# Kernel tuning notes

Measured on AMD Instinct MI355X. Metric: run time of the kernel, lower is better.

## Reference

```python
import jax, jax.numpy as jnp
import numpy as np

ALPHA = 0.2  # LeakyReLU negative slope
N1, N2, D_IN, D_OUT = 4096, 8192, 256, 256


def _xavier(key, shape):
    fan_in, fan_out = shape[0], shape[1]
    std = 1.414 * (2.0 / (fan_in + fan_out)) ** 0.5
    return (jax.random.normal(key, shape) * std).astype(jnp.float32)


def setup_inputs() -> dict:
    key = jax.random.key(0)
    k1, k2, k3, k4, k5 = jax.random.split(key, 5)
    x = jax.random.normal(k1, (N2, D_IN), dtype=jnp.float32)
    adj = (jax.random.uniform(k2, (N1, N2)) < 0.01).astype(jnp.float32)
    adj = adj.at[:, 0].set(1.0)
    weight_v2e = _xavier(k3, (D_IN, D_OUT))
    weight_e2v = _xavier(k4, (D_OUT, D_OUT))
    a = _xavier(k5, (1, 2 * D_OUT))
    return {"x": x, "adj": adj, "weight_v2e": weight_v2e, "weight_e2v": weight_e2v, "a": a}


def reference(x, adj, weight_v2e, weight_e2v, a):
    out = weight_v2e.shape[1]
    x_4att = x @ weight_v2e                              # [N2, out]
    degree = jnp.sum(adj, axis=1, keepdims=True)         # [N1, 1]
    edge = (adj @ x_4att) / degree                       # [N1, out] mean of incident node feats
    edge_4att = edge @ weight_e2v                        # [N1, out]
    # score(i,j) = a . concat(x_4att[j], edge_4att[i]); decomposes additively
    a_node = a[0, :out]                                  # applied to x_4att
    a_edge = a[0, out:]                                  # applied to edge_4att
    scores = edge_4att @ a_edge                          # [N1]
    scores = scores[:, None] + (x_4att @ a_node)[None, :]  # [N1, N2]
    pair_e = jax.nn.leaky_relu(scores, negative_slope=ALPHA)
    attention = jnp.where(adj > 0, pair_e, jnp.float32(-9e15))
    attention_node = jax.nn.softmax(attention.T, axis=1)  # [N2, N1] softmax over hyperedges per node
    node = attention_node @ edge_4att                    # [N2, out]
    return jax.nn.leaky_relu(node, negative_slope=ALPHA)
```

## Files before the change

kernel.cpp:

```cpp
#include <hip/hip_runtime.h>
#include <math.h>


#define N1 4096
#define N2 8192
#define D  256
#define ALPHA 0.2f
#define CCAP 96

__global__ void __launch_bounds__(256) prep_kernel(
    const float* __restrict__ Wv, const float* __restrict__ We,
    const float* __restrict__ a, float* __restrict__ Wf,
    float* __restrict__ vnode, float* __restrict__ vedge,
    float* __restrict__ c0num, float* __restrict__ c0den,
    int* __restrict__ colcnt)
{
    __shared__ float tmp[256];
    const int t = threadIdx.x;
    const int b = blockIdx.x;
    if (b < 256) {
        float acc = 0.f;
        for (int m = 0; m < 256; ++m)
            acc += Wv[b * 256 + m] * We[m * 256 + t];
        Wf[b * 256 + t] = acc;
    } else if (b == 256) {
        float acc = 0.f;
        for (int n = 0; n < 256; ++n)
            acc += Wv[t * 256 + n] * a[n];
        vnode[t] = acc;
        float t2 = 0.f;
        for (int n = 0; n < 256; ++n)
            t2 += We[t * 256 + n] * a[256 + n];
        tmp[t] = t2;
        __syncthreads();
        float v = 0.f;
        for (int n = 0; n < 256; ++n)
            v += Wv[t * 256 + n] * tmp[n];
        vedge[t] = v;
    } else {
        c0num[t] = 0.f;
        if (t == 0) *c0den = 0.f;
        for (int u = 0; u < 32; ++u) colcnt[u * 256 + t] = 0;
    }
}

__global__ void __launch_bounds__(512) edge_mean_kernel(
    const float* __restrict__ adj, const float* __restrict__ x,
    const float* __restrict__ vedge, float* __restrict__ ex,
    float* __restrict__ sr, int* __restrict__ colcnt,
    unsigned short* __restrict__ colidx)
{
    __shared__ int    lst[512];
    __shared__ int    cnt;
    __shared__ float4 part[7][64];
    const int t = threadIdx.x, lane = t & 63, w = t >> 6;
    const int i = blockIdx.x;
    if (t == 0) cnt = 0;
    __syncthreads();

    const float4* arow = (const float4*)(adj + (size_t)i * N2);
    for (int u = 0; u < 4; ++u) {
        const float4 v = arow[u * 512 + t];
        const int jb = (u * 512 + t) * 4;
        const float comp[4] = {v.x, v.y, v.z, v.w};
#pragma unroll
        for (int q = 0; q < 4; ++q) {
            if (comp[q] != 0.f) {
                const int k = atomicAdd(&cnt, 1);
                if (k < 512) lst[k] = jb + q;
            }
        }
    }
    __syncthreads();
    const int deg = cnt;
    const int c = deg < 512 ? deg : 512;

    for (int k = t; k < c; k += 512) {
        const int j = lst[k];
        if (j != 0) {
            const int kk = atomicAdd(&colcnt[j], 1);
            if (kk < CCAP) colidx[(size_t)j * CCAP + kk] = (unsigned short)i;
        }
    }

    const float4* x4 = (const float4*)x;
    float4 acc = {0.f, 0.f, 0.f, 0.f};
    float4 acc2 = {0.f, 0.f, 0.f, 0.f};
    int k = w;
    for (; k + 56 < c; k += 64) {
        const int j0 = lst[k],      j1 = lst[k + 8],  j2 = lst[k + 16], j3 = lst[k + 24];
        const int j4 = lst[k + 32], j5 = lst[k + 40], j6 = lst[k + 48], j7 = lst[k + 56];
        const float4 v0 = x4[(size_t)j0 * 64 + lane];
        const float4 v1 = x4[(size_t)j1 * 64 + lane];
        const float4 v2 = x4[(size_t)j2 * 64 + lane];
        const float4 v3 = x4[(size_t)j3 * 64 + lane];
        const float4 v4 = x4[(size_t)j4 * 64 + lane];
        const float4 v5 = x4[(size_t)j5 * 64 + lane];
        const float4 v6 = x4[(size_t)j6 * 64 + lane];
        const float4 v7 = x4[(size_t)j7 * 64 + lane];
        acc.x  += (v0.x + v1.x) + (v2.x + v3.x);
        acc.y  += (v0.y + v1.y) + (v2.y + v3.y);
        acc.z  += (v0.z + v1.z) + (v2.z + v3.z);
        acc.w  += (v0.w + v1.w) + (v2.w + v3.w);
        acc2.x += (v4.x + v5.x) + (v6.x + v7.x);
        acc2.y += (v4.y + v5.y) + (v6.y + v7.y);
        acc2.z += (v4.z + v5.z) + (v6.z + v7.z);
        acc2.w += (v4.w + v5.w) + (v6.w + v7.w);
    }
    for (; k + 8 < c; k += 16) {
        const float4 v0 = x4[(size_t)lst[k] * 64 + lane];
        const float4 v1 = x4[(size_t)lst[k + 8] * 64 + lane];
        acc.x += v0.x;  acc.y += v0.y;  acc.z += v0.z;  acc.w += v0.w;
        acc2.x += v1.x; acc2.y += v1.y; acc2.z += v1.z; acc2.w += v1.w;
    }
    for (; k < c; k += 8) {
        const float4 v = x4[(size_t)lst[k] * 64 + lane];
        acc.x += v.x; acc.y += v.y; acc.z += v.z; acc.w += v.w;
    }
    acc.x += acc2.x; acc.y += acc2.y; acc.z += acc2.z; acc.w += acc2.w;

    if (w > 0) part[w - 1][lane] = acc;
    __syncthreads();

    if (w == 0) {
        float4 s = acc;
#pragma unroll
        for (int p = 0; p < 7; ++p) {
            const float4 q = part[p][lane];
            s.x += q.x; s.y += q.y; s.z += q.z; s.w += q.w;
        }
        const float invd = 1.0f / (float)(deg > 0 ? deg : 1);
        float4 e = {s.x * invd, s.y * invd, s.z * invd, s.w * invd};
        ((float4*)(ex + (size_t)i * D))[lane] = e;

        const float4 ve = ((const float4*)vedge)[lane];
        float p = e.x * ve.x + e.y * ve.y + e.z * ve.z + e.w * ve.w;
#pragma unroll
        for (int off = 32; off >= 1; off >>= 1) p += __shfl_xor(p, off, 64);
        if (lane == 0) sr[i] = p;
    }
}

__global__ void __launch_bounds__(256) gemm16_kernel(
    float* __restrict__ exe, const float* __restrict__ Wf)
{
    __shared__ float exl[16 * 256];
    __shared__ float Wfl[64 * 256];
    const int t = threadIdx.x;
    const int r0 = blockIdx.x * 16;

    for (int r = 0; r < 16; ++r)
        exl[r * 256 + t] = exe[(size_t)(r0 + r) * D + t];

    float acc[16];
#pragma unroll
    for (int r = 0; r < 16; ++r) acc[r] = 0.f;

    for (int p = 0; p < 4; ++p) {
        __syncthreads();
        const float4* Wg = (const float4*)(Wf + p * 64 * 256);
        float4* Wd = (float4*)Wfl;
        for (int u = 0; u < 16; ++u)
            Wd[u * 256 + t] = Wg[u * 256 + t];
        __syncthreads();
        for (int n = 0; n < 64; ++n) {
            const float wl = Wfl[n * 256 + t];
#pragma unroll
            for (int r = 0; r < 16; ++r)
                acc[r] += exl[r * 256 + p * 64 + n] * wl;
        }
    }
#pragma unroll
    for (int r = 0; r < 16; ++r)
        exe[(size_t)(r0 + r) * D + t] = acc[r];
}

__global__ void __launch_bounds__(512) attn_kernel(
    const float* __restrict__ x, const float* __restrict__ vnode,
    const float* __restrict__ sr, const float* __restrict__ e4a,
    const int* __restrict__ colcnt, const unsigned short* __restrict__ colidx,
    float* __restrict__ out)
{
    const int t = threadIdx.x, lane = t & 63, w = t >> 6;
    const int j = blockIdx.x * 8 + w;
    if (j == 0) return;
    const float4 vn = *(const float4*)(vnode + lane * 4);
    const float4* e44 = (const float4*)e4a;

    const float4 xu = *(const float4*)(x + (size_t)j * D + lane * 4);
    float p = xu.x * vn.x + xu.y * vn.y + xu.z * vn.z + xu.w * vn.w;
#pragma unroll
    for (int off = 32; off >= 1; off >>= 1) p += __shfl_xor(p, off, 64);
    const float sc = p;

    int c = colcnt[j]; if (c > CCAP) c = CCAP;
    const unsigned short* lp = colidx + (size_t)j * CCAP;

    int   id0 = 0,  id1 = 0;
    float wk0 = 0.f, wk1 = 0.f;
    if (lane < c) {
        id0 = lp[lane];
        float s = sr[id0] + sc;
        s = s > 0.f ? s : ALPHA * s;
        wk0 = __expf(s);
    }
    if (lane + 64 < c) {
        id1 = lp[lane + 64];
        float s = sr[id1] + sc;
        s = s > 0.f ? s : ALPHA * s;
        wk1 = __expf(s);
    }
    float den = wk0 + wk1;
#pragma unroll
    for (int off = 32; off >= 1; off >>= 1) den += __shfl_xor(den, off, 64);

    float4 acc = {0.f, 0.f, 0.f, 0.f};
    float4 accB = {0.f, 0.f, 0.f, 0.f};
    const int c1 = c < 64 ? c : 64;
    int k = 0;
    for (; k + 7 < c1; k += 8) {
        const int   i0 = __shfl(id0, k, 64),     i1 = __shfl(id0, k + 1, 64);
        const int   i2 = __shfl(id0, k + 2, 64), i3 = __shfl(id0, k + 3, 64);
        const int   i4 = __shfl(id0, k + 4, 64), i5 = __shfl(id0, k + 5, 64);
        const int   i6 = __shfl(id0, k + 6, 64), i7 = __shfl(id0, k + 7, 64);
        const float w0 = __shfl(wk0, k, 64),     w1 = __shfl(wk0, k + 1, 64);
        const float w2 = __shfl(wk0, k + 2, 64), w3 = __shfl(wk0, k + 3, 64);
        const float w4 = __shfl(wk0, k + 4, 64), w5 = __shfl(wk0, k + 5, 64);
        const float w6 = __shfl(wk0, k + 6, 64), w7 = __shfl(wk0, k + 7, 64);
        const float4 v0 = e44[(size_t)i0 * 64 + lane];
        const float4 v1 = e44[(size_t)i1 * 64 + lane];
        const float4 v2 = e44[(size_t)i2 * 64 + lane];
        const float4 v3 = e44[(size_t)i3 * 64 + lane];
        const float4 v4 = e44[(size_t)i4 * 64 + lane];
        const float4 v5 = e44[(size_t)i5 * 64 + lane];
        const float4 v6 = e44[(size_t)i6 * 64 + lane];
        const float4 v7 = e44[(size_t)i7 * 64 + lane];
        acc.x  += w0 * v0.x + w1 * v1.x + w2 * v2.x + w3 * v3.x;
        acc.y  += w0 * v0.y + w1 * v1.y + w2 * v2.y + w3 * v3.y;
        acc.z  += w0 * v0.z + w1 * v1.z + w2 * v2.z + w3 * v3.z;
        acc.w  += w0 * v0.w + w1 * v1.w + w2 * v2.w + w3 * v3.w;
        accB.x += w4 * v4.x + w5 * v5.x + w6 * v6.x + w7 * v7.x;
        accB.y += w4 * v4.y + w5 * v5.y + w6 * v6.y + w7 * v7.y;
        accB.z += w4 * v4.z + w5 * v5.z + w6 * v6.z + w7 * v7.z;
        accB.w += w4 * v4.w + w5 * v5.w + w6 * v6.w + w7 * v7.w;
    }
    for (; k < c1; ++k) {
        const int   idx = __shfl(id0, k, 64);
        const float wt  = __shfl(wk0, k, 64);
        const float4 v = e44[(size_t)idx * 64 + lane];
        acc.x += wt * v.x; acc.y += wt * v.y; acc.z += wt * v.z; acc.w += wt * v.w;
    }
    for (k = 64; k < c; ++k) {
        const int   idx = __shfl(id1, k - 64, 64);
        const float wt  = __shfl(wk1, k - 64, 64);
        const float4 v = e44[(size_t)idx * 64 + lane];
        accB.x += wt * v.x; accB.y += wt * v.y; accB.z += wt * v.z; accB.w += wt * v.w;
    }
    acc.x += accB.x; acc.y += accB.y; acc.z += accB.z; acc.w += accB.w;

    const float dinv = den > 0.f ? 1.0f / den : 0.f;
    float n0 = acc.x * dinv, n1 = acc.y * dinv, n2 = acc.z * dinv, n3 = acc.w * dinv;
    n0 = n0 > 0.f ? n0 : ALPHA * n0;
    n1 = n1 > 0.f ? n1 : ALPHA * n1;
    n2 = n2 > 0.f ? n2 : ALPHA * n2;
    n3 = n3 > 0.f ? n3 : ALPHA * n3;
    const float4 o = {n0, n1, n2, n3};
    *(float4*)(out + (size_t)j * D + lane * 4) = o;
}

__global__ void __launch_bounds__(256) col0_partial_kernel(
    const float* __restrict__ x, const float* __restrict__ vnode,
    const float* __restrict__ sr, const float* __restrict__ e4a,
    float* __restrict__ c0num, float* __restrict__ c0den)
{
    __shared__ float red[256];
    __shared__ float wl[16];
    const int t = threadIdx.x;
    const int r0 = blockIdx.x * 16;

    red[t] = x[t] * vnode[t];
    __syncthreads();
    for (int s = 128; s > 0; s >>= 1) {
        if (t < s) red[t] += red[t + s];
        __syncthreads();
    }
    const float sc0 = red[0];
    __syncthreads();

    if (t < 16) {
        float s = sr[r0 + t] + sc0;
        s = s > 0.f ? s : ALPHA * s;
        wl[t] = __expf(s);
    }
    __syncthreads();

    float num = 0.f;
#pragma unroll
    for (int r = 0; r < 16; ++r)
        num += wl[r] * e4a[(size_t)(r0 + r) * D + t];
    atomicAdd(&c0num[t], num);
    if (t == 0) {
        float ds = 0.f;
#pragma unroll
        for (int r = 0; r < 16; ++r) ds += wl[r];
        atomicAdd(c0den, ds);
    }
}

__global__ void __launch_bounds__(256) col0_final_kernel(
    const float* __restrict__ c0num, const float* __restrict__ c0den,
    float* __restrict__ out)
{
    const int t = threadIdx.x;
    const float d = *c0den;
    float v = d > 0.f ? c0num[t] / d : 0.f;
    out[t] = v > 0.f ? v : ALPHA * v;
}

extern "C" void kernel_launch(void* const* d_in, const int* in_sizes, int n_in,
                              void* d_out, int out_size, void* d_ws, size_t ws_size,
                              hipStream_t stream)
{
    const float* x   = (const float*)d_in[0];
    const float* adj = (const float*)d_in[1];
    const float* Wv  = (const float*)d_in[2];
    const float* We  = (const float*)d_in[3];
    const float* a   = (const float*)d_in[4];

    char* ws = (char*)d_ws;
    float*          exe4a  = (float*)(ws);
    float*          sr     = (float*)(ws + 0x400000);
    float*          Wf     = (float*)(ws + 0x404000);
    float*          vnode  = (float*)(ws + 0x444000);
    float*          vedge  = (float*)(ws + 0x444400);
    float*          c0num  = (float*)(ws + 0x444800);
    float*          c0den  = (float*)(ws + 0x444C00);
    int*            colcnt = (int*)(ws + 0x444D00);
    unsigned short* colidx = (unsigned short*)(ws + 0x44CD00);

    prep_kernel<<<dim3(258), dim3(256), 0, stream>>>(Wv, We, a, Wf, vnode, vedge,
                                                     c0num, c0den, colcnt);
    edge_mean_kernel<<<dim3(N1), dim3(512), 0, stream>>>(adj, x, vedge, exe4a, sr,
                                                         colcnt, colidx);
    gemm16_kernel<<<dim3(N1 / 16), dim3(256), 0, stream>>>(exe4a, Wf);
    attn_kernel<<<dim3(N2 / 8), dim3(512), 0, stream>>>(x, vnode, sr, exe4a,
                                                        colcnt, colidx, (float*)d_out);
    col0_partial_kernel<<<dim3(256), dim3(256), 0, stream>>>(x, vnode, sr, exe4a,
                                                             c0num, c0den);
    col0_final_kernel<<<dim3(1), dim3(256), 0, stream>>>(c0num, c0den, (float*)d_out);
}
```

Baseline: 308.6 us.

## Split adjacency scan from edge gather and use wave-ballot compaction

The fused edge-mean kernel is split into a lightweight scan kernel that compacts each adjacency row's nonzero indices into a global row list, and a gather kernel that reads that list and averages x rows. The scan uses wavefront ballot/popcount to replace per-element shared atomics with one atomic per wave, and does the column-index atomics inline. The intent is to cut shared-atomic contention and let the bandwidth-bound scan and the gather run at separate occupancy. The cost is an extra launch plus writing and reading the row index list through global memory.

```diff
diff --git a/kernel.cpp b/kernel.cpp
--- a/kernel.cpp
+++ b/kernel.cpp
@@ -7,6 +7,7 @@
 #define D  256
 #define ALPHA 0.2f
 #define CCAP 96
+#define RCAP 512
 
 __global__ void __launch_bounds__(256) prep_kernel(
     const float* __restrict__ Wv, const float* __restrict__ We,
@@ -44,44 +45,64 @@
     }
 }
 
-__global__ void __launch_bounds__(512) edge_mean_kernel(
-    const float* __restrict__ adj, const float* __restrict__ x,
-    const float* __restrict__ vedge, float* __restrict__ ex,
-    float* __restrict__ sr, int* __restrict__ colcnt,
+__global__ void __launch_bounds__(256) scan_kernel(
+    const float* __restrict__ adj, int* __restrict__ rowcnt,
+    unsigned short* __restrict__ rowidx, int* __restrict__ colcnt,
     unsigned short* __restrict__ colidx)
 {
-    __shared__ int    lst[512];
-    __shared__ int    cnt;
+    __shared__ int cnt;
+    const int t = threadIdx.x, lane = t & 63;
+    const int i = blockIdx.x;
+    if (t == 0) cnt = 0;
+    __syncthreads();
+
+    const float4* arow = (const float4*)(adj + (size_t)i * N2);
+    unsigned short* rp = rowidx + (size_t)i * RCAP;
+
+    for (int u = 0; u < 8; ++u) {
+        const float4 v = arow[u * 256 + t];
+        const int jb = (u * 256 + t) * 4;
+        const float comp[4] = {v.x, v.y, v.z, v.w};
+#pragma unroll
+        for (int q = 0; q < 4; ++q) {
+            const bool nz = (comp[q] != 0.f);
+            const unsigned long long m = __ballot(nz);
+            if (m) {
+                int base = 0;
+                if (lane == 0) base = atomicAdd(&cnt, __popcll(m));
+                base = __shfl(base, 0, 64);
+                if (nz) {
+                    const int j = jb + q;
+                    const int pos = base +
+                        __popcll(m & ((1ull << lane) - 1ull));
+                    if (pos < RCAP) rp[pos] = (unsigned short)j;
+                    if (j != 0) {
+                        const int kk = atomicAdd(&colcnt[j], 1);
+                        if (kk < CCAP)
+                            colidx[(size_t)j * CCAP + kk] = (unsigned short)i;
+                    }
+                }
+            }
+        }
+    }
+    __syncthreads();
+    if (t == 0) rowcnt[i] = cnt;
+}
+
+__global__ void __launch_bounds__(512) edge_gather_kernel(
+    const float* __restrict__ x, const int* __restrict__ rowcnt,
+    const unsigned short* __restrict__ rowidx, const float* __restrict__ vedge,
+    float* __restrict__ ex, float* __restrict__ sr)
+{
+    __shared__ unsigned short lst[RCAP];
     __shared__ float4 part[7][64];
     const int t = threadIdx.x, lane = t & 63, w = t >> 6;
     const int i = blockIdx.x;
-    if (t == 0) cnt = 0;
-    __syncthreads();
-
-    const float4* arow = (const float4*)(adj + (size_t)i * N2);
-    for (int u = 0; u < 4; ++u) {
-        const float4 v = arow[u * 512 + t];
-        const int jb = (u * 512 + t) * 4;
-        const float comp[4] = {v.x, v.y, v.z, v.w};
-#pragma unroll
-        for (int q = 0; q < 4; ++q) {
-            if (comp[q] != 0.f) {
-                const int k = atomicAdd(&cnt, 1);
-                if (k < 512) lst[k] = jb + q;
-            }
-        }
-    }
-    __syncthreads();
-    const int deg = cnt;
-    const int c = deg < 512 ? deg : 512;
-
-    for (int k = t; k < c; k += 512) {
-        const int j = lst[k];
-        if (j != 0) {
-            const int kk = atomicAdd(&colcnt[j], 1);
-            if (kk < CCAP) colidx[(size_t)j * CCAP + kk] = (unsigned short)i;
-        }
-    }
+
+    const int deg = rowcnt[i];
+    const int c = deg < RCAP ? deg : RCAP;
+    if (t < c) lst[t] = rowidx[(size_t)i * RCAP + t];
+    __syncthreads();
 
     const float4* x4 = (const float4*)x;
     float4 acc = {0.f, 0.f, 0.f, 0.f};
@@ -337,11 +358,15 @@
     float*          c0den  = (float*)(ws + 0x444C00);
     int*            colcnt = (int*)(ws + 0x444D00);
     unsigned short* colidx = (unsigned short*)(ws + 0x44CD00);
+    int*            rowcnt = (int*)(ws + 0x5CCD00);
+    unsigned short* rowidx = (unsigned short*)(ws + 0x5D0D00);
 
     prep_kernel<<<dim3(258), dim3(256), 0, stream>>>(Wv, We, a, Wf, vnode, vedge,
                                                      c0num, c0den, colcnt);
-    edge_mean_kernel<<<dim3(N1), dim3(512), 0, stream>>>(adj, x, vedge, exe4a, sr,
-                                                         colcnt, colidx);
+    scan_kernel<<<dim3(N1), dim3(256), 0, stream>>>(adj, rowcnt, rowidx,
+                                                    colcnt, colidx);
+    edge_gather_kernel<<<dim3(N1), dim3(512), 0, stream>>>(x, rowcnt, rowidx,
+                                                           vedge, exe4a, sr);
     gemm16_kernel<<<dim3(N1 / 16), dim3(256), 0, stream>>>(exe4a, Wf);
     attn_kernel<<<dim3(N2 / 8), dim3(512), 0, stream>>>(x, vnode, sr, exe4a,
                                                         colcnt, colidx, (float*)d_out);
```

After: 332.4 us. +7.7%, slower.

## Replace sparse column gather attention with dense bf16 MFMA GEMM over adjacency

Applied to the files above, without the earlier changes.

Drops the per-column sparse index lists (colcnt/colidx built with atomics), the separate column-0 path and the per-node gather of edge features. The node aggregation becomes a dense GEMM: softmax weights are computed on the fly from the adjacency tile, packed to bf16, and multiplied against a transposed bf16 copy of edge_4att with MFMA 16x16x32 instructions, with the denominator accumulated in shared memory. This re-reads the full 128MB adjacency and does dense work over roughly 99% zeros, and it adds bf16 rounding error, in exchange for regular, tensor-core-friendly access.

```diff
diff --git a/kernel.cpp b/kernel.cpp
--- a/kernel.cpp
+++ b/kernel.cpp
@@ -6,14 +6,20 @@
 #define N2 8192
 #define D  256
 #define ALPHA 0.2f
-#define CCAP 96
+
+typedef __attribute__((ext_vector_type(8))) short short8;
+typedef __attribute__((ext_vector_type(4))) float floatx4;
+
+__device__ __forceinline__ unsigned short f2b(float f) {
+    unsigned int x = __float_as_uint(f);
+    x += 0x7FFFu + ((x >> 16) & 1u);
+    return (unsigned short)(x >> 16);
+}
 
 __global__ void __launch_bounds__(256) prep_kernel(
     const float* __restrict__ Wv, const float* __restrict__ We,
     const float* __restrict__ a, float* __restrict__ Wf,
-    float* __restrict__ vnode, float* __restrict__ vedge,
-    float* __restrict__ c0num, float* __restrict__ c0den,
-    int* __restrict__ colcnt)
+    float* __restrict__ vnode, float* __restrict__ vedge)
 {
     __shared__ float tmp[256];
     const int t = threadIdx.x;
@@ -23,7 +29,7 @@
         for (int m = 0; m < 256; ++m)
             acc += Wv[b * 256 + m] * We[m * 256 + t];
         Wf[b * 256 + t] = acc;
-    } else if (b == 256) {
+    } else {
         float acc = 0.f;
         for (int n = 0; n < 256; ++n)
             acc += Wv[t * 256 + n] * a[n];
@@ -37,18 +43,13 @@
         for (int n = 0; n < 256; ++n)
             v += Wv[t * 256 + n] * tmp[n];
         vedge[t] = v;
-    } else {
-        c0num[t] = 0.f;
-        if (t == 0) *c0den = 0.f;
-        for (int u = 0; u < 32; ++u) colcnt[u * 256 + t] = 0;
     }
 }
 
 __global__ void __launch_bounds__(512) edge_mean_kernel(
     const float* __restrict__ adj, const float* __restrict__ x,
     const float* __restrict__ vedge, float* __restrict__ ex,
-    float* __restrict__ sr, int* __restrict__ colcnt,
-    unsigned short* __restrict__ colidx)
+    float* __restrict__ sr)
 {
     __shared__ int    lst[512];
     __shared__ int    cnt;
@@ -74,14 +75,6 @@
     __syncthreads();
     const int deg = cnt;
     const int c = deg < 512 ? deg : 512;
-
-    for (int k = t; k < c; k += 512) {
-        const int j = lst[k];
-        if (j != 0) {
-            const int kk = atomicAdd(&colcnt[j], 1);
-            if (kk < CCAP) colidx[(size_t)j * CCAP + kk] = (unsigned short)i;
-        }
-    }
 
     const float4* x4 = (const float4*)x;
     float4 acc = {0.f, 0.f, 0.f, 0.f};
@@ -142,7 +135,8 @@
 }
 
 __global__ void __launch_bounds__(256) gemm16_kernel(
-    float* __restrict__ exe, const float* __restrict__ Wf)
+    const float* __restrict__ ex, const float* __restrict__ Wf,
+    unsigned short* __restrict__ e4aT)
 {
     __shared__ float exl[16 * 256];
     __shared__ float Wfl[64 * 256];
@@ -150,7 +144,7 @@
     const int r0 = blockIdx.x * 16;
 
     for (int r = 0; r < 16; ++r)
-        exl[r * 256 + t] = exe[(size_t)(r0 + r) * D + t];
+        exl[r * 256 + t] = ex[(size_t)(r0 + r) * D + t];
 
     float acc[16];
 #pragma unroll
@@ -170,151 +164,134 @@
                 acc[r] += exl[r * 256 + p * 64 + n] * wl;
         }
     }
-#pragma unroll
-    for (int r = 0; r < 16; ++r)
-        exe[(size_t)(r0 + r) * D + t] = acc[r];
-}
-
-__global__ void __launch_bounds__(512) attn_kernel(
+    unsigned short pk[16];
+#pragma unroll
+    for (int r = 0; r < 16; ++r) pk[r] = f2b(acc[r]);
+    unsigned short* dst = e4aT + (size_t)t * N1 + r0;
+    *(uint4*)(dst)     = *(const uint4*)(&pk[0]);
+    *(uint4*)(dst + 8) = *(const uint4*)(&pk[8]);
+}
+
+__global__ void __launch_bounds__(512) sc_kernel(
     const float* __restrict__ x, const float* __restrict__ vnode,
-    const float* __restrict__ sr, const float* __restrict__ e4a,
-    const int* __restrict__ colcnt, const unsigned short* __restrict__ colidx,
-    float* __restrict__ out)
+    float* __restrict__ sc)
 {
     const int t = threadIdx.x, lane = t & 63, w = t >> 6;
     const int j = blockIdx.x * 8 + w;
-    if (j == 0) return;
     const float4 vn = *(const float4*)(vnode + lane * 4);
-    const float4* e44 = (const float4*)e4a;
-
     const float4 xu = *(const float4*)(x + (size_t)j * D + lane * 4);
     float p = xu.x * vn.x + xu.y * vn.y + xu.z * vn.z + xu.w * vn.w;
 #pragma unroll
     for (int off = 32; off >= 1; off >>= 1) p += __shfl_xor(p, off, 64);
-    const float sc = p;
-
-    int c = colcnt[j]; if (c > CCAP) c = CCAP;
-    const unsigned short* lp = colidx + (size_t)j * CCAP;
-
-    int   id0 = 0,  id1 = 0;
-    float wk0 = 0.f, wk1 = 0.f;
-    if (lane < c) {
-        id0 = lp[lane];
-        float s = sr[id0] + sc;
-        s = s > 0.f ? s : ALPHA * s;
-        wk0 = __expf(s);
-    }
-    if (lane + 64 < c) {
-        id1 = lp[lane + 64];
-        float s = sr[id1] + sc;
-        s = s > 0.f ? s : ALPHA * s;
-        wk1 = __expf(s);
-    }
-    float den = wk0 + wk1;
-#pragma unroll
-    for (int off = 32; off >= 1; off >>= 1) den += __shfl_xor(den, off, 64);
-
-    float4 acc = {0.f, 0.f, 0.f, 0.f};
-    float4 accB = {0.f, 0.f, 0.f, 0.f};
-    const int c1 = c < 64 ? c : 64;
-    int k = 0;
-    for (; k + 7 < c1; k += 8) {
-        const int   i0 = __shfl(id0, k, 64),     i1 = __shfl(id0, k + 1, 64);
-        const int   i2 = __shfl(id0, k + 2, 64), i3 = __shfl(id0, k + 3, 64);
-        const int   i4 = __shfl(id0, k + 4, 64), i5 = __shfl(id0, k + 5, 64);
-        const int   i6 = __shfl(id0, k + 6, 64), i7 = __shfl(id0, k + 7, 64);
-        const float w0 = __shfl(wk0, k, 64),     w1 = __shfl(wk0, k + 1, 64);
-        const float w2 = __shfl(wk0, k + 2, 64), w3 = __shfl(wk0, k + 3, 64);
-        const float w4 = __shfl(wk0, k + 4, 64), w5 = __shfl(wk0, k + 5, 64);
-        const float w6 = __shfl(wk0, k + 6, 64), w7 = __shfl(wk0, k + 7, 64);
-        const float4 v0 = e44[(size_t)i0 * 64 + lane];
-        const float4 v1 = e44[(size_t)i1 * 64 + lane];
-        const float4 v2 = e44[(size_t)i2 * 64 + lane];
-        const float4 v3 = e44[(size_t)i3 * 64 + lane];
-        const float4 v4 = e44[(size_t)i4 * 64 + lane];
-        const float4 v5 = e44[(size_t)i5 * 64 + lane];
-        const float4 v6 = e44[(size_t)i6 * 64 + lane];
-        const float4 v7 = e44[(size_t)i7 * 64 + lane];
-        acc.x  += w0 * v0.x + w1 * v1.x + w2 * v2.x + w3 * v3.x;
-        acc.y  += w0 * v0.y + w1 * v1.y + w2 * v2.y + w3 * v3.y;
-        acc.z  += w0 * v0.z + w1 * v1.z + w2 * v2.z + w3 * v3.z;
-        acc.w  += w0 * v0.w + w1 * v1.w + w2 * v2.w + w3 * v3.w;
-        accB.x += w4 * v4.x + w5 * v5.x + w6 * v6.x + w7 * v7.x;
-        accB.y += w4 * v4.y + w5 * v5.y + w6 * v6.y + w7 * v7.y;
-        accB.z += w4 * v4.z + w5 * v5.z + w6 * v6.z + w7 * v7.z;
-        accB.w += w4 * v4.w + w5 * v5.w + w6 * v6.w + w7 * v7.w;
-    }
-    for (; k < c1; ++k) {
-        const int   idx = __shfl(id0, k, 64);
-        const float wt  = __shfl(wk0, k, 64);
-        const float4 v = e44[(size_t)idx * 64 + lane];
-        acc.x += wt * v.x; acc.y += wt * v.y; acc.z += wt * v.z; acc.w += wt * v.w;
-    }
-    for (k = 64; k < c; ++k) {
-        const int   idx = __shfl(id1, k - 64, 64);
-        const float wt  = __shfl(wk1, k - 64, 64);
-        const float4 v = e44[(size_t)idx * 64 + lane];
-        accB.x += wt * v.x; accB.y += wt * v.y; accB.z += wt * v.z; accB.w += wt * v.w;
-    }
-    acc.x += accB.x; acc.y += accB.y; acc.z += accB.z; acc.w += accB.w;
-
-    const float dinv = den > 0.f ? 1.0f / den : 0.f;
-    float n0 = acc.x * dinv, n1 = acc.y * dinv, n2 = acc.z * dinv, n3 = acc.w * dinv;
-    n0 = n0 > 0.f ? n0 : ALPHA * n0;
-    n1 = n1 > 0.f ? n1 : ALPHA * n1;
-    n2 = n2 > 0.f ? n2 : ALPHA * n2;
-    n3 = n3 > 0.f ? n3 : ALPHA * n3;
-    const float4 o = {n0, n1, n2, n3};
-    *(float4*)(out + (size_t)j * D + lane * 4) = o;
-}
-
-__global__ void __launch_bounds__(256) col0_partial_kernel(
-    const float* __restrict__ x, const float* __restrict__ vnode,
-    const float* __restrict__ sr, const float* __restrict__ e4a,
-    float* __restrict__ c0num, float* __restrict__ c0den)
-{
-    __shared__ float red[256];
-    __shared__ float wl[16];
-    const int t = threadIdx.x;
-    const int r0 = blockIdx.x * 16;
-
-    red[t] = x[t] * vnode[t];
-    __syncthreads();
-    for (int s = 128; s > 0; s >>= 1) {
-        if (t < s) red[t] += red[t + s];
-        __syncthreads();
-    }
-    const float sc0 = red[0];
-    __syncthreads();
-
-    if (t < 16) {
-        float s = sr[r0 + t] + sc0;
-        s = s > 0.f ? s : ALPHA * s;
-        wl[t] = __expf(s);
-    }
-    __syncthreads();
-
-    float num = 0.f;
-#pragma unroll
-    for (int r = 0; r < 16; ++r)
-        num += wl[r] * e4a[(size_t)(r0 + r) * D + t];
-    atomicAdd(&c0num[t], num);
-    if (t == 0) {
-        float ds = 0.f;
-#pragma unroll
-        for (int r = 0; r < 16; ++r) ds += wl[r];
-        atomicAdd(c0den, ds);
-    }
-}
-
-__global__ void __launch_bounds__(256) col0_final_kernel(
-    const float* __restrict__ c0num, const float* __restrict__ c0den,
+    if (lane == 0) sc[j] = p;
+}
+
+__global__ void __launch_bounds__(512) gemm2_kernel(
+    const float* __restrict__ adj, const float* __restrict__ sr,
+    const float* __restrict__ sc, const unsigned short* __restrict__ e4aT,
     float* __restrict__ out)
 {
-    const int t = threadIdx.x;
-    const float d = *c0den;
-    float v = d > 0.f ? c0num[t] / d : 0.f;
-    out[t] = v > 0.f ? v : ALPHA * v;
+    __shared__ unsigned short A_w[32 * 64];
+    __shared__ unsigned short BT[256 * 64];
+    __shared__ float scl[32];
+    __shared__ float den_l[32];
+    const int t = threadIdx.x, lane = t & 63, w = t >> 6;
+    const int j0 = blockIdx.x * 32;
+
+    if (t < 32) { scl[t] = sc[j0 + t]; den_l[t] = 0.f; }
+
+    const int jown   = t & 31;
+    const int islice = t >> 5;
+    const int iq     = islice >> 1;
+    const int ebase  = (islice & 1) * 4;
+    float den_reg = 0.f;
+
+    const int bc   = t >> 1;
+    const int bh   = t & 1;
+
+    floatx4 acc0 = {0.f,0.f,0.f,0.f}, acc1 = {0.f,0.f,0.f,0.f};
+    floatx4 acc2 = {0.f,0.f,0.f,0.f}, acc3 = {0.f,0.f,0.f,0.f};
+
+    const int mt  = w & 1;
+    const int nt0 = (w >> 1) * 4;
+    const int fm  = mt * 16 + (lane & 15);
+    const int fl7 = lane & 7;
+    const int fq  = lane >> 4;
+
+    __syncthreads();
+
+    for (int kt = 0; kt < 64; ++kt) {
+        const int k0 = kt * 64;
+
+        {
+            const float scj = scl[jown];
+            unsigned short pk[4];
+#pragma unroll
+            for (int u = 0; u < 4; ++u) {
+                const int i = islice * 4 + u;
+                const float av = adj[(size_t)(k0 + i) * N2 + j0 + jown];
+                float wv = 0.f;
+                if (av != 0.f) {
+                    float s = sr[k0 + i] + scj;
+                    s = s > 0.f ? s : ALPHA * s;
+                    s = fminf(fmaxf(s, -60.f), 60.f);
+                    wv = __expf(s);
+                }
+                den_reg += wv;
+                pk[u] = f2b(wv);
+            }
+            *(ushort4*)&A_w[jown * 64 + (iq ^ (jown & 7)) * 8 + ebase] =
+                *(const ushort4*)pk;
+        }
+        {
+            const unsigned short* src = e4aT + (size_t)bc * N1 + k0 + bh * 32;
+            unsigned short* drow = &BT[bc * 64];
+            const int c7 = bc & 7;
+#pragma unroll
+            for (int m = 0; m < 4; ++m) {
+                const uint4 v = *(const uint4*)(src + m * 8);
+                *(uint4*)&drow[((bh * 4 + m) ^ c7) * 8] = v;
+            }
+        }
+        __syncthreads();
+
+#pragma unroll
+        for (int step = 0; step < 2; ++step) {
+            const int kq = step * 4 + fq;
+            const short8 af =
+                *(const short8*)&A_w[fm * 64 + (kq ^ fl7) * 8];
+            const short8 b0 =
+                *(const short8*)&BT[((nt0 + 0) * 16 + (lane & 15)) * 64 + (kq ^ fl7) * 8];
+            const short8 b1 =
+                *(const short8*)&BT[((nt0 + 1) * 16 + (lane & 15)) * 64 + (kq ^ fl7) * 8];
+            const short8 b2 =
+                *(const short8*)&BT[((nt0 + 2) * 16 + (lane & 15)) * 64 + (kq ^ fl7) * 8];
+            const short8 b3 =
+                *(const short8*)&BT[((nt0 + 3) * 16 + (lane & 15)) * 64 + (kq ^ fl7) * 8];
+            acc0 = __builtin_amdgcn_mfma_f32_16x16x32_bf16(af, b0, acc0, 0, 0, 0);
+            acc1 = __builtin_amdgcn_mfma_f32_16x16x32_bf16(af, b1, acc1, 0, 0, 0);
+            acc2 = __builtin_amdgcn_mfma_f32_16x16x32_bf16(af, b2, acc2, 0, 0, 0);
+            acc3 = __builtin_amdgcn_mfma_f32_16x16x32_bf16(af, b3, acc3, 0, 0, 0);
+        }
+        __syncthreads();
+    }
+
+    atomicAdd(&den_l[jown], den_reg);
+    __syncthreads();
+
+    const floatx4 accs[4] = {acc0, acc1, acc2, acc3};
+#pragma unroll
+    for (int p = 0; p < 4; ++p) {
+        const int cg = (nt0 + p) * 16 + (lane & 15);
+#pragma unroll
+        for (int r = 0; r < 4; ++r) {
+            const int jl = mt * 16 + fq * 4 + r;
+            const float dv = den_l[jl];
+            float v = dv > 0.f ? accs[p][r] / dv : 0.f;
+            v = v > 0.f ? v : ALPHA * v;
+            out[(size_t)(j0 + jl) * D + cg] = v;
+        }
+    }
 }
 
 extern "C" void kernel_launch(void* const* d_in, const int* in_sizes, int n_in,
@@ -328,24 +305,18 @@
     const float* a   = (const float*)d_in[4];
 
     char* ws = (char*)d_ws;
-    float*          exe4a  = (float*)(ws);
-    float*          sr     = (float*)(ws + 0x400000);
-    float*          Wf     = (float*)(ws + 0x404000);
-    float*          vnode  = (float*)(ws + 0x444000);
-    float*          vedge  = (float*)(ws + 0x444400);
-    float*          c0num  = (float*)(ws + 0x444800);
-    float*          c0den  = (float*)(ws + 0x444C00);
-    int*            colcnt = (int*)(ws + 0x444D00);
-    unsigned short* colidx = (unsigned short*)(ws + 0x44CD00);
-
-    prep_kernel<<<dim3(258), dim3(256), 0, stream>>>(Wv, We, a, Wf, vnode, vedge,
-                                                     c0num, c0den, colcnt);
-    edge_mean_kernel<<<dim3(N1), dim3(512), 0, stream>>>(adj, x, vedge, exe4a, sr,
-                                                         colcnt, colidx);
-    gemm16_kernel<<<dim3(N1 / 16), dim3(256), 0, stream>>>(exe4a, Wf);
-    attn_kernel<<<dim3(N2 / 8), dim3(512), 0, stream>>>(x, vnode, sr, exe4a,
-                                                        colcnt, colidx, (float*)d_out);
-    col0_partial_kernel<<<dim3(256), dim3(256), 0, stream>>>(x, vnode, sr, exe4a,
-                                                             c0num, c0den);
-    col0_final_kernel<<<dim3(1), dim3(256), 0, stream>>>(c0num, c0den, (float*)d_out);
-}
+    float*          ex    = (float*)(ws);
+    float*          sr    = (float*)(ws + 0x400000);
+    float*          Wf    = (float*)(ws + 0x404000);
+    float*          vnode = (float*)(ws + 0x444000);
+    float*          vedge = (float*)(ws + 0x444400);
+    float*          sc    = (float*)(ws + 0x444800);
+    unsigned short* e4aT  = (unsigned short*)(ws + 0x500000);
+
+    prep_kernel<<<dim3(257), dim3(256), 0, stream>>>(Wv, We, a, Wf, vnode, vedge);
+    edge_mean_kernel<<<dim3(N1), dim3(512), 0, stream>>>(adj, x, vedge, ex, sr);
+    gemm16_kernel<<<dim3(N1 / 16), dim3(256), 0, stream>>>(ex, Wf, e4aT);
+    sc_kernel<<<dim3(N2 / 8), dim3(512), 0, stream>>>(x, vnode, sc);
+    gemm2_kernel<<<dim3(N2 / 32), dim3(512), 0, stream>>>(adj, sr, sc, e4aT,
+                                                          (float*)d_out);
+}
```

Result: slower. 414.1 us (+34.2%).
